# Optimization experiments

Measured on AMD Instinct MI355X. Metric: run time of the kernel, lower is better.

## Reference

```python
import jax, jax.numpy as jnp
import numpy as np

D_MODEL = 1024
N_HEADS = 16
D_HEAD = D_MODEL // N_HEADS
LN_EPS = 1e-5


def setup_inputs() -> dict:
    key = jax.random.key(0)
    ks = jax.random.split(key, 10)
    B, N = 2, 2048
    s = 1.0 / np.sqrt(D_MODEL)
    return {
        "x": jax.random.normal(ks[0], (B, N, D_MODEL), dtype=jnp.float32),
        "Wq": jax.random.normal(ks[1], (D_MODEL, D_MODEL), dtype=jnp.float32) * s,
        "bq": jnp.zeros((D_MODEL,), dtype=jnp.float32),
        "Wk": jax.random.normal(ks[2], (D_MODEL, D_MODEL), dtype=jnp.float32) * s,
        "bk": jnp.zeros((D_MODEL,), dtype=jnp.float32),
        "Wv": jax.random.normal(ks[3], (D_MODEL, D_MODEL), dtype=jnp.float32) * s,
        "bv": jnp.zeros((D_MODEL,), dtype=jnp.float32),
        "Wo": jax.random.normal(ks[4], (D_MODEL, D_MODEL), dtype=jnp.float32) * s,
        "bo": jnp.zeros((D_MODEL,), dtype=jnp.float32),
        "ln_gamma": jnp.ones((D_MODEL,), dtype=jnp.float32),
        "ln_beta": jnp.zeros((D_MODEL,), dtype=jnp.float32),
    }


def reference(x, Wq, bq, Wk, bk, Wv, bv, Wo, bo, ln_gamma, ln_beta):
    B, N, _ = x.shape
    # QKV projections -> [B, H, N, dh]
    def proj(W, b):
        return (x @ W.T + b).reshape(B, N, N_HEADS, D_HEAD).transpose(0, 2, 1, 3)
    Q, K, V = proj(Wq, bq), proj(Wk, bk), proj(Wv, bv)
    # scaled scores [B, H, N, N] with causal mask (is_mask=True)
    scores = jnp.einsum("bhqd,bhkd->bhqk", Q, K) / np.sqrt(D_HEAD)
    causal = jnp.tril(jnp.ones((N, N), dtype=bool))
    scores = jnp.where(causal, scores, -jnp.inf)
    attn = jax.nn.softmax(scores, axis=-1)  # dropout p=0 (eval)
    ctx = jnp.einsum("bhqk,bhkd->bhqd", attn, V)  # [B, H, N, dh]
    ctx = ctx.transpose(0, 2, 1, 3).reshape(B, N, D_MODEL)
    out = ctx @ Wo.T + bo + x  # output proj + residual
    # LayerNorm over last dim
    mu = out.mean(-1, keepdims=True)
    var = out.var(-1, keepdims=True)
    return (out - mu) / jnp.sqrt(var + LN_EPS) * ln_gamma + ln_beta
```

## Files before the change

kernel.cpp:

```cpp
#include <hip/hip_runtime.h>
#include <type_traits>

#define D_MODEL 1024
#define NHEADS 16
#define DHEAD 64
#define SEQ 2048
#define BATCH 2
#define MROWS (BATCH*SEQ)
#define NQT (SEQ/64)

typedef unsigned short ushort_t;
using bf16x8 = __attribute__((ext_vector_type(8))) __bf16;
using us4    = __attribute__((ext_vector_type(4))) unsigned short;
using us8    = __attribute__((ext_vector_type(8))) unsigned short;
using f32x4  = __attribute__((ext_vector_type(4))) float;

__device__ __forceinline__ ushort_t f2bf(float f) {
    unsigned int u = __builtin_bit_cast(unsigned int, f);
    u += 0x7FFFu + ((u >> 16) & 1u);
    return (ushort_t)(u >> 16);
}

__device__ __forceinline__ void gl2lds(const ushort_t* g, ushort_t* l) {
    __builtin_amdgcn_global_load_lds(
        (const __attribute__((address_space(1))) unsigned int*)g,
        (__attribute__((address_space(3))) unsigned int*)l,
        16, 0, 0);
}

__global__ __launch_bounds__(256) void cvt_kernel(
    const float* __restrict__ x,
    const float* __restrict__ wq, const float* __restrict__ wk,
    const float* __restrict__ wv, const float* __restrict__ wo,
    ushort_t* __restrict__ xb,
    ushort_t* __restrict__ wqb, ushort_t* __restrict__ wkb,
    ushort_t* __restrict__ wvb, ushort_t* __restrict__ wob)
{
    const size_t XN = (size_t)MROWS * D_MODEL;
    const size_t WN = (size_t)D_MODEL * D_MODEL;
    size_t i = ((size_t)blockIdx.x * 256 + threadIdx.x) * 4;
    const float* s; ushort_t* d; size_t off;
    if (i < XN) { s = x; d = xb; off = i; }
    else {
        size_t j = i - XN;
        int w = (int)(j / WN);
        off = j - (size_t)w * WN;
        s = (w == 0) ? wq : (w == 1) ? wk : (w == 2) ? wv : wo;
        d = (w == 0) ? wqb : (w == 1) ? wkb : (w == 2) ? wvb : wob;
    }
    const f32x4 v = *(const f32x4*)(s + off);
    us4 o;
    #pragma unroll
    for (int t = 0; t < 4; ++t) o[t] = f2bf(v[t]);
    *(us4*)(d + off) = o;
}

template<typename OutT, bool RES>
__global__ __launch_bounds__(256, 3) void gemm_nt(
    const ushort_t* __restrict__ A,
    const ushort_t* __restrict__ W0, const ushort_t* __restrict__ W1, const ushort_t* __restrict__ W2,
    const float* __restrict__ b0, const float* __restrict__ b1, const float* __restrict__ b2,
    const float* __restrict__ res,
    OutT* __restrict__ Y0, OutT* __restrict__ Y1, OutT* __restrict__ Y2)
{
    constexpr int K  = D_MODEL;
    constexpr int BK = 32;
    __shared__ ushort_t As[128 * BK];
    __shared__ ushort_t Ws[128 * BK];

    const int z = blockIdx.z;
    const ushort_t* W  = (z == 0) ? W0 : (z == 1) ? W1 : W2;
    const float* bias  = (z == 0) ? b0 : (z == 1) ? b1 : b2;
    OutT* Y            = (z == 0) ? Y0 : (z == 1) ? Y1 : Y2;

    const int i0 = blockIdx.x * 128;
    const int j0 = blockIdx.y * 128;
    const int tid  = threadIdx.x;
    const int lane = tid & 63;
    const int w    = tid >> 6;
    const int wm   = (w >> 1) * 64;
    const int wn   = (w & 1) * 64;
    const int l15  = lane & 15;
    const int quad = lane >> 4;

    const int srow = lane >> 2;
    const int scol = (lane & 3) * 8;
    const int c0 = w * 2, c1 = w * 2 + 1;
    const ushort_t* gA0 = A + (size_t)(i0 + c0 * 16 + srow) * K + scol;
    const ushort_t* gA1 = A + (size_t)(i0 + c1 * 16 + srow) * K + scol;
    const ushort_t* gW0 = W + (size_t)(j0 + c0 * 16 + srow) * K + scol;
    const ushort_t* gW1 = W + (size_t)(j0 + c1 * 16 + srow) * K + scol;
    ushort_t* lA0 = As + c0 * 512;
    ushort_t* lA1 = As + c1 * 512;
    ushort_t* lW0 = Ws + c0 * 512;
    ushort_t* lW1 = Ws + c1 * 512;

    f32x4 acc[4][4] = {};

    for (int k0 = 0; k0 < K; k0 += BK) {
        gl2lds(gA0 + k0, lA0);
        gl2lds(gA1 + k0, lA1);
        gl2lds(gW0 + k0, lW0);
        gl2lds(gW1 + k0, lW1);
        __syncthreads();

        bf16x8 af[4], wf[4];
        #pragma unroll
        for (int m = 0; m < 4; ++m)
            af[m] = *(const bf16x8*)&As[(wm + m * 16 + l15) * BK + quad * 8];
        #pragma unroll
        for (int n = 0; n < 4; ++n)
            wf[n] = *(const bf16x8*)&Ws[(wn + n * 16 + l15) * BK + quad * 8];
        #pragma unroll
        for (int m = 0; m < 4; ++m)
            #pragma unroll
            for (int n = 0; n < 4; ++n)
                acc[m][n] = __builtin_amdgcn_mfma_f32_16x16x32_bf16(af[m], wf[n], acc[m][n], 0, 0, 0);
        __syncthreads();
    }

    #pragma unroll
    for (int n = 0; n < 4; ++n) {
        const int col = j0 + wn + n * 16 + l15;
        const float bv = bias[col];
        #pragma unroll
        for (int m = 0; m < 4; ++m) {
            #pragma unroll
            for (int r = 0; r < 4; ++r) {
                const int row = i0 + wm + m * 16 + quad * 4 + r;
                float v = acc[m][n][r] + bv;
                if constexpr (RES) v += res[(size_t)row * D_MODEL + col];
                if constexpr (std::is_same<OutT, float>::value)
                    Y[(size_t)row * D_MODEL + col] = v;
                else
                    Y[(size_t)row * D_MODEL + col] = f2bf(v);
            }
        }
    }
}

#define VP 72

__global__ __launch_bounds__(256, 3) void attn_kernel(
    const ushort_t* __restrict__ Qg, const ushort_t* __restrict__ Kg,
    const ushort_t* __restrict__ Vg, ushort_t* __restrict__ Og)
{
    __shared__ ushort_t Kt[2][64 * VP];
    __shared__ ushort_t Vt[2][64 * VP];
    __shared__ ushort_t Pw[64 * VP];
    __shared__ ushort_t OnesR[16 * VP];

    const int bh = blockIdx.y;
    const int b = bh >> 4;
    const int h = bh & 15;
    const int p = blockIdx.x;
    const int tid  = threadIdx.x;
    const int lane = tid & 63;
    const int w    = tid >> 6;
    const int l15  = lane & 15;
    const int quad = lane >> 4;

    const size_t headoff = (size_t)h * DHEAD;
    const ushort_t* Kbase = Kg + (size_t)(b * SEQ) * D_MODEL + headoff;
    const ushort_t* Vbase = Vg + (size_t)(b * SEQ) * D_MODEL + headoff;

    const int krow = tid >> 3;
    const int kb   = tid & 7;
    const int vkey = tid & 63;
    const int dc0  = tid >> 6;
    const int dc1  = dc0 + 4;

    for (int i = tid; i < 16 * VP; i += 256) OnesR[i] = 0x3F80;

    bf16x8 onesf[2];
    bool onesLoaded = false;

    for (int half = 0; half < 2; ++half) {
        const int qt = half ? p : (NQT - 1 - p);
        const int q0 = qt * 64;
        const int qg = q0 + w * 16 + l15;
        const int nkt = qt + 1;

        const size_t qrow = (size_t)(b * SEQ + qg) * D_MODEL + headoff;
        const bf16x8 qf0 = *(const bf16x8*)&Qg[qrow + quad * 8];
        const bf16x8 qf1 = *(const bf16x8*)&Qg[qrow + 32 + quad * 8];

        float m_run = -1e30f;
        f32x4 o[4] = {};
        f32x4 o4 = {};

        us8 kp0, kp1, vp0, vp1;
        kp0 = *(const us8*)&Kbase[(size_t)krow * D_MODEL + kb * 8];
        kp1 = *(const us8*)&Kbase[(size_t)(32 + krow) * D_MODEL + kb * 8];
        vp0 = *(const us8*)&Vbase[(size_t)vkey * D_MODEL + dc0 * 8];
        vp1 = *(const us8*)&Vbase[(size_t)vkey * D_MODEL + dc1 * 8];
        *(us8*)&Kt[0][krow * VP + kb * 8]        = kp0;
        *(us8*)&Kt[0][(32 + krow) * VP + kb * 8] = kp1;
        #pragma unroll
        for (int j = 0; j < 8; ++j) {
            Vt[0][(dc0 * 8 + j) * VP + vkey] = vp0[j];
            Vt[0][(dc1 * 8 + j) * VP + vkey] = vp1[j];
        }
        __syncthreads();

        if (!onesLoaded) {
            onesf[0] = *(const bf16x8*)&OnesR[l15 * VP + quad * 8];
            onesf[1] = *(const bf16x8*)&OnesR[l15 * VP + 32 + quad * 8];
            onesLoaded = true;
        }

        for (int kt = 0; kt < nkt; ++kt) {
            const int cur = kt & 1;
            const int nxt = cur ^ 1;
            const bool pre = (kt + 1 < nkt);
            if (pre) {
                const size_t koff = (size_t)((kt + 1) * 64) * D_MODEL;
                kp0 = *(const us8*)&Kbase[koff + (size_t)krow * D_MODEL + kb * 8];
                kp1 = *(const us8*)&Kbase[koff + (size_t)(32 + krow) * D_MODEL + kb * 8];
                vp0 = *(const us8*)&Vbase[koff + (size_t)vkey * D_MODEL + dc0 * 8];
                vp1 = *(const us8*)&Vbase[koff + (size_t)vkey * D_MODEL + dc1 * 8];
            }

            f32x4 sv[4];
            #pragma unroll
            for (int f = 0; f < 4; ++f) {
                const bf16x8 kf0 = *(const bf16x8*)&Kt[cur][(f * 16 + l15) * VP + quad * 8];
                const bf16x8 kf1 = *(const bf16x8*)&Kt[cur][(f * 16 + l15) * VP + 32 + quad * 8];
                f32x4 s = {};
                s = __builtin_amdgcn_mfma_f32_16x16x32_bf16(kf0, qf0, s, 0, 0, 0);
                s = __builtin_amdgcn_mfma_f32_16x16x32_bf16(kf1, qf1, s, 0, 0, 0);
                sv[f] = s;
            }

            if (kt * 64 + 63 <= q0 + w * 16) {
                #pragma unroll
                for (int f = 0; f < 4; ++f)
                    #pragma unroll
                    for (int r = 0; r < 4; ++r) sv[f][r] *= 0.125f;
            } else {
                #pragma unroll
                for (int f = 0; f < 4; ++f) {
                    #pragma unroll
                    for (int r = 0; r < 4; ++r) {
                        const int kg = kt * 64 + f * 16 + quad * 4 + r;
                        sv[f][r] = (kg <= qg) ? sv[f][r] * 0.125f : -1e30f;
                    }
                }
            }

            float mf[4];
            #pragma unroll
            for (int f = 0; f < 4; ++f)
                mf[f] = fmaxf(fmaxf(sv[f][0], sv[f][1]), fmaxf(sv[f][2], sv[f][3]));
            float mx = fmaxf(fmaxf(mf[0], mf[1]), fmaxf(mf[2], mf[3]));
            mx = fmaxf(mx, __shfl_xor(mx, 16));
            mx = fmaxf(mx, __shfl_xor(mx, 32));
            const float mn = fmaxf(m_run, mx);
            const float al = __expf(m_run - mn);
            m_run = mn;
            #pragma unroll
            for (int f = 0; f < 4; ++f)
                #pragma unroll
                for (int r = 0; r < 4; ++r) sv[f][r] = __expf(sv[f][r] - mn);

            #pragma unroll
            for (int t = 0; t < 4; ++t)
                #pragma unroll
                for (int r = 0; r < 4; ++r) o[t][r] *= al;
            #pragma unroll
            for (int r = 0; r < 4; ++r) o4[r] *= al;

            #pragma unroll
            for (int f = 0; f < 4; ++f) {
                us4 pk;
                #pragma unroll
                for (int r = 0; r < 4; ++r) pk[r] = f2bf(sv[f][r]);
                *(us4*)&Pw[(w * 16 + l15) * VP + f * 16 + quad * 4] = pk;
            }
            __asm__ volatile("s_waitcnt lgkmcnt(0)" ::: "memory");

            #pragma unroll
            for (int s = 0; s < 2; ++s) {
                const bf16x8 pf = *(const bf16x8*)&Pw[(w * 16 + l15) * VP + s * 32 + quad * 8];
                #pragma unroll
                for (int t = 0; t < 4; ++t) {
                    const bf16x8 vf = *(const bf16x8*)&Vt[cur][(t * 16 + l15) * VP + s * 32 + quad * 8];
                    o[t] = __builtin_amdgcn_mfma_f32_16x16x32_bf16(vf, pf, o[t], 0, 0, 0);
                }
                o4 = __builtin_amdgcn_mfma_f32_16x16x32_bf16(onesf[s], pf, o4, 0, 0, 0);
            }

            if (pre) {
                *(us8*)&Kt[nxt][krow * VP + kb * 8]        = kp0;
                *(us8*)&Kt[nxt][(32 + krow) * VP + kb * 8] = kp1;
                #pragma unroll
                for (int j = 0; j < 8; ++j) {
                    Vt[nxt][(dc0 * 8 + j) * VP + vkey] = vp0[j];
                    Vt[nxt][(dc1 * 8 + j) * VP + vkey] = vp1[j];
                }
            }
            __asm__ volatile("s_waitcnt lgkmcnt(0)\n\ts_barrier" ::: "memory");
        }

        const float inv = 1.f / o4[0];
        const size_t orow = (size_t)(b * SEQ + q0 + w * 16 + l15) * D_MODEL + headoff;
        #pragma unroll
        for (int t = 0; t < 4; ++t) {
            us4 pk;
            #pragma unroll
            for (int r = 0; r < 4; ++r) pk[r] = f2bf(o[t][r] * inv);
            *(us4*)&Og[orow + t * 16 + quad * 4] = pk;
        }
    }
}

__global__ __launch_bounds__(256) void ln_kernel(
    const float* __restrict__ X, const float* __restrict__ g,
    const float* __restrict__ bta, float* __restrict__ out)
{
    __shared__ float r1[4], r2[4];
    const int row = blockIdx.x;
    const int tid = threadIdx.x;
    const float* p = X + (size_t)row * D_MODEL;
    float v[4]; float s1 = 0.f, s2 = 0.f;
    #pragma unroll
    for (int i = 0; i < 4; ++i) { v[i] = p[tid + 256 * i]; s1 += v[i]; s2 += v[i] * v[i]; }
    #pragma unroll
    for (int d = 32; d >= 1; d >>= 1) { s1 += __shfl_xor(s1, d); s2 += __shfl_xor(s2, d); }
    if ((tid & 63) == 0) { r1[tid >> 6] = s1; r2[tid >> 6] = s2; }
    __syncthreads();
    s1 = r1[0] + r1[1] + r1[2] + r1[3];
    s2 = r2[0] + r2[1] + r2[2] + r2[3];
    const float mu  = s1 * (1.f / D_MODEL);
    const float var = s2 * (1.f / D_MODEL) - mu * mu;
    const float rstd = rsqrtf(var + 1e-5f);
    #pragma unroll
    for (int i = 0; i < 4; ++i) {
        const int c = tid + 256 * i;
        out[(size_t)row * D_MODEL + c] = (v[i] - mu) * rstd * g[c] + bta[c];
    }
}

extern "C" void kernel_launch(void* const* d_in, const int* in_sizes, int n_in,
                              void* d_out, int out_size, void* d_ws, size_t ws_size,
                              hipStream_t stream) {
    const float* x     = (const float*)d_in[0];
    const float* Wq    = (const float*)d_in[1];
    const float* bq    = (const float*)d_in[2];
    const float* Wk    = (const float*)d_in[3];
    const float* bk    = (const float*)d_in[4];
    const float* Wv    = (const float*)d_in[5];
    const float* bv    = (const float*)d_in[6];
    const float* Wo    = (const float*)d_in[7];
    const float* bo    = (const float*)d_in[8];
    const float* gamma = (const float*)d_in[9];
    const float* beta  = (const float*)d_in[10];

    const size_t XN = (size_t)MROWS * D_MODEL;
    const size_t WN = (size_t)D_MODEL * D_MODEL;
    ushort_t* wsp = (ushort_t*)d_ws;
    ushort_t* xb  = wsp;
    ushort_t* Yq  = wsp + XN;
    ushort_t* Yk  = wsp + 2 * XN;
    ushort_t* Yv  = wsp + 3 * XN;
    ushort_t* Wqb = wsp + 4 * XN;
    ushort_t* Wkb = Wqb + WN;
    ushort_t* Wvb = Wkb + WN;
    ushort_t* Wob = Wvb + WN;
    ushort_t* ctx = xb;
    float*    pre = (float*)d_out;

    cvt_kernel<<<dim3(8192), 256, 0, stream>>>(x, Wq, Wk, Wv, Wo, xb, Wqb, Wkb, Wvb, Wob);

    gemm_nt<ushort_t, false><<<dim3(MROWS / 128, D_MODEL / 128, 3), 256, 0, stream>>>(
        xb, Wqb, Wkb, Wvb, bq, bk, bv, nullptr, Yq, Yk, Yv);

    attn_kernel<<<dim3(SEQ / 128, BATCH * NHEADS), 256, 0, stream>>>(Yq, Yk, Yv, ctx);

    gemm_nt<float, true><<<dim3(MROWS / 128, D_MODEL / 128, 1), 256, 0, stream>>>(
        ctx, Wob, Wob, Wob, bo, bo, bo, x, pre, pre, pre);

    ln_kernel<<<dim3(MROWS), 256, 0, stream>>>(pre, gamma, beta, (float*)d_out);
}
```

Baseline: 220.4 us.

## Process two key tiles per attention iteration with shared online-softmax rescale

Restructures the causal attention inner loop to handle two 64-key tiles per iteration. It computes both QK tiles, applies one max and rescale over both, then runs both PV products, and prefetches the next two tiles into registers. This halves the per-tile softmax rescale and reduction work and gives more independent MFMA work between barriers. In exchange it doubles the prefetch register footprint and adds a second barrier per iteration, which may cut occupancy under the launch bound of 3 blocks.

Measured after the change: 221.3 us. About the same (+0.4%).

```diff
diff --git a/kernel.cpp b/kernel.cpp
--- a/kernel.cpp
+++ b/kernel.cpp
@@ -141,13 +141,75 @@
 
 #define VP 72
 
+__device__ __forceinline__ void qk_tile(
+    const ushort_t* Ktb, const bf16x8& qf0, const bf16x8& qf1,
+    int l15, int quad, f32x4* sv)
+{
+    #pragma unroll
+    for (int f = 0; f < 4; ++f) {
+        const bf16x8 kf0 = *(const bf16x8*)&Ktb[(f * 16 + l15) * VP + quad * 8];
+        const bf16x8 kf1 = *(const bf16x8*)&Ktb[(f * 16 + l15) * VP + 32 + quad * 8];
+        f32x4 s = {};
+        s = __builtin_amdgcn_mfma_f32_16x16x32_bf16(kf0, qf0, s, 0, 0, 0);
+        s = __builtin_amdgcn_mfma_f32_16x16x32_bf16(kf1, qf1, s, 0, 0, 0);
+        sv[f] = s;
+    }
+}
+
+__device__ __forceinline__ void mask_scale(f32x4* sv, int kt, int q0w, int qg, int quad)
+{
+    if (kt * 64 + 63 <= q0w) {
+        #pragma unroll
+        for (int f = 0; f < 4; ++f)
+            #pragma unroll
+            for (int r = 0; r < 4; ++r) sv[f][r] *= 0.125f;
+    } else {
+        #pragma unroll
+        for (int f = 0; f < 4; ++f) {
+            #pragma unroll
+            for (int r = 0; r < 4; ++r) {
+                const int kg = kt * 64 + f * 16 + quad * 4 + r;
+                sv[f][r] = (kg <= qg) ? sv[f][r] * 0.125f : -1e30f;
+            }
+        }
+    }
+}
+
+__device__ __forceinline__ void pack_p(const f32x4* sv, ushort_t* PwX, int row, int quad)
+{
+    #pragma unroll
+    for (int f = 0; f < 4; ++f) {
+        us4 pk;
+        #pragma unroll
+        for (int r = 0; r < 4; ++r) pk[r] = f2bf(sv[f][r]);
+        *(us4*)&PwX[row * VP + f * 16 + quad * 4] = pk;
+    }
+}
+
+__device__ __forceinline__ void pv_tile(
+    const ushort_t* PwX, const ushort_t* Vtb, const bf16x8* onesf,
+    int row, int l15, int quad, f32x4 (&o)[4], f32x4& o4)
+{
+    #pragma unroll
+    for (int s = 0; s < 2; ++s) {
+        const bf16x8 pf = *(const bf16x8*)&PwX[row * VP + s * 32 + quad * 8];
+        #pragma unroll
+        for (int t = 0; t < 4; ++t) {
+            const bf16x8 vf = *(const bf16x8*)&Vtb[(t * 16 + l15) * VP + s * 32 + quad * 8];
+            o[t] = __builtin_amdgcn_mfma_f32_16x16x32_bf16(vf, pf, o[t], 0, 0, 0);
+        }
+        o4 = __builtin_amdgcn_mfma_f32_16x16x32_bf16(onesf[s], pf, o4, 0, 0, 0);
+    }
+}
+
 __global__ __launch_bounds__(256, 3) void attn_kernel(
     const ushort_t* __restrict__ Qg, const ushort_t* __restrict__ Kg,
     const ushort_t* __restrict__ Vg, ushort_t* __restrict__ Og)
 {
     __shared__ ushort_t Kt[2][64 * VP];
     __shared__ ushort_t Vt[2][64 * VP];
-    __shared__ ushort_t Pw[64 * VP];
+    __shared__ ushort_t Pw0[64 * VP];
+    __shared__ ushort_t Pw1[64 * VP];
     __shared__ ushort_t OnesR[16 * VP];
 
     const int bh = blockIdx.y;
@@ -172,6 +234,8 @@
 
     for (int i = tid; i < 16 * VP; i += 256) OnesR[i] = 0x3F80;
 
+    const int prow = w * 16 + l15;
+
     bf16x8 onesf[2];
     bool onesLoaded = false;
 
@@ -179,6 +243,7 @@
         const int qt = half ? p : (NQT - 1 - p);
         const int q0 = qt * 64;
         const int qg = q0 + w * 16 + l15;
+        const int q0w = q0 + w * 16;
         const int nkt = qt + 1;
 
         const size_t qrow = (size_t)(b * SEQ + qg) * D_MODEL + headoff;
@@ -189,17 +254,32 @@
         f32x4 o[4] = {};
         f32x4 o4 = {};
 
-        us8 kp0, kp1, vp0, vp1;
-        kp0 = *(const us8*)&Kbase[(size_t)krow * D_MODEL + kb * 8];
-        kp1 = *(const us8*)&Kbase[(size_t)(32 + krow) * D_MODEL + kb * 8];
-        vp0 = *(const us8*)&Vbase[(size_t)vkey * D_MODEL + dc0 * 8];
-        vp1 = *(const us8*)&Vbase[(size_t)vkey * D_MODEL + dc1 * 8];
-        *(us8*)&Kt[0][krow * VP + kb * 8]        = kp0;
-        *(us8*)&Kt[0][(32 + krow) * VP + kb * 8] = kp1;
-        #pragma unroll
-        for (int j = 0; j < 8; ++j) {
-            Vt[0][(dc0 * 8 + j) * VP + vkey] = vp0[j];
-            Vt[0][(dc1 * 8 + j) * VP + vkey] = vp1[j];
+        {
+            us8 k0 = *(const us8*)&Kbase[(size_t)krow * D_MODEL + kb * 8];
+            us8 k1 = *(const us8*)&Kbase[(size_t)(32 + krow) * D_MODEL + kb * 8];
+            us8 v0 = *(const us8*)&Vbase[(size_t)vkey * D_MODEL + dc0 * 8];
+            us8 v1 = *(const us8*)&Vbase[(size_t)vkey * D_MODEL + dc1 * 8];
+            *(us8*)&Kt[0][krow * VP + kb * 8]        = k0;
+            *(us8*)&Kt[0][(32 + krow) * VP + kb * 8] = k1;
+            #pragma unroll
+            for (int j = 0; j < 8; ++j) {
+                Vt[0][(dc0 * 8 + j) * VP + vkey] = v0[j];
+                Vt[0][(dc1 * 8 + j) * VP + vkey] = v1[j];
+            }
+            if (nkt > 1) {
+                const size_t koff = (size_t)64 * D_MODEL;
+                k0 = *(const us8*)&Kbase[koff + (size_t)krow * D_MODEL + kb * 8];
+                k1 = *(const us8*)&Kbase[koff + (size_t)(32 + krow) * D_MODEL + kb * 8];
+                v0 = *(const us8*)&Vbase[koff + (size_t)vkey * D_MODEL + dc0 * 8];
+                v1 = *(const us8*)&Vbase[koff + (size_t)vkey * D_MODEL + dc1 * 8];
+                *(us8*)&Kt[1][krow * VP + kb * 8]        = k0;
+                *(us8*)&Kt[1][(32 + krow) * VP + kb * 8] = k1;
+                #pragma unroll
+                for (int j = 0; j < 8; ++j) {
+                    Vt[1][(dc0 * 8 + j) * VP + vkey] = v0[j];
+                    Vt[1][(dc1 * 8 + j) * VP + vkey] = v1[j];
+                }
+            }
         }
         __syncthreads();
 
@@ -209,50 +289,38 @@
             onesLoaded = true;
         }
 
-        for (int kt = 0; kt < nkt; ++kt) {
-            const int cur = kt & 1;
-            const int nxt = cur ^ 1;
-            const bool pre = (kt + 1 < nkt);
-            if (pre) {
-                const size_t koff = (size_t)((kt + 1) * 64) * D_MODEL;
-                kp0 = *(const us8*)&Kbase[koff + (size_t)krow * D_MODEL + kb * 8];
-                kp1 = *(const us8*)&Kbase[koff + (size_t)(32 + krow) * D_MODEL + kb * 8];
-                vp0 = *(const us8*)&Vbase[koff + (size_t)vkey * D_MODEL + dc0 * 8];
-                vp1 = *(const us8*)&Vbase[koff + (size_t)vkey * D_MODEL + dc1 * 8];
-            }
-
-            f32x4 sv[4];
+        int kt = 0;
+        while (kt + 1 < nkt) {
+            const bool p0 = (kt + 2 < nkt);
+            const bool p1 = (kt + 3 < nkt);
+            us8 ka0, ka1, va0, va1, kb0_, kb1_, vb0, vb1;
+            if (p0) {
+                const size_t koff = (size_t)((kt + 2) * 64) * D_MODEL;
+                ka0 = *(const us8*)&Kbase[koff + (size_t)krow * D_MODEL + kb * 8];
+                ka1 = *(const us8*)&Kbase[koff + (size_t)(32 + krow) * D_MODEL + kb * 8];
+                va0 = *(const us8*)&Vbase[koff + (size_t)vkey * D_MODEL + dc0 * 8];
+                va1 = *(const us8*)&Vbase[koff + (size_t)vkey * D_MODEL + dc1 * 8];
+            }
+            if (p1) {
+                const size_t koff = (size_t)((kt + 3) * 64) * D_MODEL;
+                kb0_ = *(const us8*)&Kbase[koff + (size_t)krow * D_MODEL + kb * 8];
+                kb1_ = *(const us8*)&Kbase[koff + (size_t)(32 + krow) * D_MODEL + kb * 8];
+                vb0  = *(const us8*)&Vbase[koff + (size_t)vkey * D_MODEL + dc0 * 8];
+                vb1  = *(const us8*)&Vbase[koff + (size_t)vkey * D_MODEL + dc1 * 8];
+            }
+
+            f32x4 sv0[4], sv1[4];
+            qk_tile(Kt[0], qf0, qf1, l15, quad, sv0);
+            qk_tile(Kt[1], qf0, qf1, l15, quad, sv1);
+            mask_scale(sv0, kt,     q0w, qg, quad);
+            mask_scale(sv1, kt + 1, q0w, qg, quad);
+
+            float mx = -1e30f;
             #pragma unroll
             for (int f = 0; f < 4; ++f) {
-                const bf16x8 kf0 = *(const bf16x8*)&Kt[cur][(f * 16 + l15) * VP + quad * 8];
-                const bf16x8 kf1 = *(const bf16x8*)&Kt[cur][(f * 16 + l15) * VP + 32 + quad * 8];
-                f32x4 s = {};
-                s = __builtin_amdgcn_mfma_f32_16x16x32_bf16(kf0, qf0, s, 0, 0, 0);
-                s = __builtin_amdgcn_mfma_f32_16x16x32_bf16(kf1, qf1, s, 0, 0, 0);
-                sv[f] = s;
-            }
-
-            if (kt * 64 + 63 <= q0 + w * 16) {
-                #pragma unroll
-                for (int f = 0; f < 4; ++f)
-                    #pragma unroll
-                    for (int r = 0; r < 4; ++r) sv[f][r] *= 0.125f;
-            } else {
-                #pragma unroll
-                for (int f = 0; f < 4; ++f) {
-                    #pragma unroll
-                    for (int r = 0; r < 4; ++r) {
-                        const int kg = kt * 64 + f * 16 + quad * 4 + r;
-                        sv[f][r] = (kg <= qg) ? sv[f][r] * 0.125f : -1e30f;
-                    }
-                }
-            }
-
-            float mf[4];
-            #pragma unroll
-            for (int f = 0; f < 4; ++f)
-                mf[f] = fmaxf(fmaxf(sv[f][0], sv[f][1]), fmaxf(sv[f][2], sv[f][3]));
-            float mx = fmaxf(fmaxf(mf[0], mf[1]), fmaxf(mf[2], mf[3]));
+                mx = fmaxf(mx, fmaxf(fmaxf(sv0[f][0], sv0[f][1]), fmaxf(sv0[f][2], sv0[f][3])));
+                mx = fmaxf(mx, fmaxf(fmaxf(sv1[f][0], sv1[f][1]), fmaxf(sv1[f][2], sv1[f][3])));
+            }
             mx = fmaxf(mx, __shfl_xor(mx, 16));
             mx = fmaxf(mx, __shfl_xor(mx, 32));
             const float mn = fmaxf(m_run, mx);
@@ -261,8 +329,10 @@
             #pragma unroll
             for (int f = 0; f < 4; ++f)
                 #pragma unroll
-                for (int r = 0; r < 4; ++r) sv[f][r] = __expf(sv[f][r] - mn);
-
+                for (int r = 0; r < 4; ++r) {
+                    sv0[f][r] = __expf(sv0[f][r] - mn);
+                    sv1[f][r] = __expf(sv1[f][r] - mn);
+                }
             #pragma unroll
             for (int t = 0; t < 4; ++t)
                 #pragma unroll
@@ -270,35 +340,63 @@
             #pragma unroll
             for (int r = 0; r < 4; ++r) o4[r] *= al;
 
-            #pragma unroll
-            for (int f = 0; f < 4; ++f) {
-                us4 pk;
-                #pragma unroll
-                for (int r = 0; r < 4; ++r) pk[r] = f2bf(sv[f][r]);
-                *(us4*)&Pw[(w * 16 + l15) * VP + f * 16 + quad * 4] = pk;
-            }
+            pack_p(sv0, Pw0, prow, quad);
+            pack_p(sv1, Pw1, prow, quad);
             __asm__ volatile("s_waitcnt lgkmcnt(0)" ::: "memory");
 
-            #pragma unroll
-            for (int s = 0; s < 2; ++s) {
-                const bf16x8 pf = *(const bf16x8*)&Pw[(w * 16 + l15) * VP + s * 32 + quad * 8];
-                #pragma unroll
-                for (int t = 0; t < 4; ++t) {
-                    const bf16x8 vf = *(const bf16x8*)&Vt[cur][(t * 16 + l15) * VP + s * 32 + quad * 8];
-                    o[t] = __builtin_amdgcn_mfma_f32_16x16x32_bf16(vf, pf, o[t], 0, 0, 0);
+            pv_tile(Pw0, Vt[0], onesf, prow, l15, quad, o, o4);
+            pv_tile(Pw1, Vt[1], onesf, prow, l15, quad, o, o4);
+
+            __asm__ volatile("s_waitcnt lgkmcnt(0)\n\ts_barrier" ::: "memory");
+
+            if (p0) {
+                *(us8*)&Kt[0][krow * VP + kb * 8]        = ka0;
+                *(us8*)&Kt[0][(32 + krow) * VP + kb * 8] = ka1;
+                #pragma unroll
+                for (int j = 0; j < 8; ++j) {
+                    Vt[0][(dc0 * 8 + j) * VP + vkey] = va0[j];
+                    Vt[0][(dc1 * 8 + j) * VP + vkey] = va1[j];
                 }
-                o4 = __builtin_amdgcn_mfma_f32_16x16x32_bf16(onesf[s], pf, o4, 0, 0, 0);
-            }
-
-            if (pre) {
-                *(us8*)&Kt[nxt][krow * VP + kb * 8]        = kp0;
-                *(us8*)&Kt[nxt][(32 + krow) * VP + kb * 8] = kp1;
+            }
+            if (p1) {
+                *(us8*)&Kt[1][krow * VP + kb * 8]        = kb0_;
+                *(us8*)&Kt[1][(32 + krow) * VP + kb * 8] = kb1_;
                 #pragma unroll
                 for (int j = 0; j < 8; ++j) {
-                    Vt[nxt][(dc0 * 8 + j) * VP + vkey] = vp0[j];
-                    Vt[nxt][(dc1 * 8 + j) * VP + vkey] = vp1[j];
+                    Vt[1][(dc0 * 8 + j) * VP + vkey] = vb0[j];
+                    Vt[1][(dc1 * 8 + j) * VP + vkey] = vb1[j];
                 }
             }
+            __asm__ volatile("s_waitcnt lgkmcnt(0)\n\ts_barrier" ::: "memory");
+            kt += 2;
+        }
+        if (kt < nkt) {
+            f32x4 sv0[4];
+            qk_tile(Kt[0], qf0, qf1, l15, quad, sv0);
+            mask_scale(sv0, kt, q0w, qg, quad);
+            float mx = -1e30f;
+            #pragma unroll
+            for (int f = 0; f < 4; ++f)
+                mx = fmaxf(mx, fmaxf(fmaxf(sv0[f][0], sv0[f][1]), fmaxf(sv0[f][2], sv0[f][3])));
+            mx = fmaxf(mx, __shfl_xor(mx, 16));
+            mx = fmaxf(mx, __shfl_xor(mx, 32));
+            const float mn = fmaxf(m_run, mx);
+            const float al = __expf(m_run - mn);
+            m_run = mn;
+            #pragma unroll
+            for (int f = 0; f < 4; ++f)
+                #pragma unroll
+                for (int r = 0; r < 4; ++r) sv0[f][r] = __expf(sv0[f][r] - mn);
+            #pragma unroll
+            for (int t = 0; t < 4; ++t)
+                #pragma unroll
+                for (int r = 0; r < 4; ++r) o[t][r] *= al;
+            #pragma unroll
+            for (int r = 0; r < 4; ++r) o4[r] *= al;
+
+            pack_p(sv0, Pw0, prow, quad);
+            __asm__ volatile("s_waitcnt lgkmcnt(0)" ::: "memory");
+            pv_tile(Pw0, Vt[0], onesf, prow, l15, quad, o, o4);
             __asm__ volatile("s_waitcnt lgkmcnt(0)\n\ts_barrier" ::: "memory");
         }
 
```

## Widen GEMM K-step to 64 and vectorize epilogue via swapped MFMA operands

Applied to the files above, without the earlier changes.

The projection GEMM now loads two 32-wide K slices per iteration, which halves the number of barrier pairs across the K loop. The MFMA operands are swapped so each lane holds four consecutive output columns of one row. That lets the epilogue issue vectorized 16-byte float stores (or 8-byte bf16 stores), vector bias loads and vector residual loads in place of scalar strided ones. LDS use doubles per block, which may reduce occupancy under the 3-blocks-per-CU launch bound.

Result: no change. 218.2 us (-1.0%).

```diff
diff --git a/kernel.cpp b/kernel.cpp
--- a/kernel.cpp
+++ b/kernel.cpp
@@ -63,10 +63,9 @@
     const float* __restrict__ res,
     OutT* __restrict__ Y0, OutT* __restrict__ Y1, OutT* __restrict__ Y2)
 {
-    constexpr int K  = D_MODEL;
-    constexpr int BK = 32;
-    __shared__ ushort_t As[128 * BK];
-    __shared__ ushort_t Ws[128 * BK];
+    constexpr int K = D_MODEL;
+    __shared__ ushort_t As[2][128 * 32];
+    __shared__ ushort_t Ws[2][128 * 32];
 
     const int z = blockIdx.z;
     const ushort_t* W  = (z == 0) ? W0 : (z == 1) ? W1 : W2;
@@ -90,50 +89,60 @@
     const ushort_t* gA1 = A + (size_t)(i0 + c1 * 16 + srow) * K + scol;
     const ushort_t* gW0 = W + (size_t)(j0 + c0 * 16 + srow) * K + scol;
     const ushort_t* gW1 = W + (size_t)(j0 + c1 * 16 + srow) * K + scol;
-    ushort_t* lA0 = As + c0 * 512;
-    ushort_t* lA1 = As + c1 * 512;
-    ushort_t* lW0 = Ws + c0 * 512;
-    ushort_t* lW1 = Ws + c1 * 512;
 
     f32x4 acc[4][4] = {};
 
-    for (int k0 = 0; k0 < K; k0 += BK) {
-        gl2lds(gA0 + k0, lA0);
-        gl2lds(gA1 + k0, lA1);
-        gl2lds(gW0 + k0, lW0);
-        gl2lds(gW1 + k0, lW1);
+    for (int k0 = 0; k0 < K; k0 += 64) {
+        gl2lds(gA0 + k0,      &As[0][c0 * 512]);
+        gl2lds(gA1 + k0,      &As[0][c1 * 512]);
+        gl2lds(gA0 + k0 + 32, &As[1][c0 * 512]);
+        gl2lds(gA1 + k0 + 32, &As[1][c1 * 512]);
+        gl2lds(gW0 + k0,      &Ws[0][c0 * 512]);
+        gl2lds(gW1 + k0,      &Ws[0][c1 * 512]);
+        gl2lds(gW0 + k0 + 32, &Ws[1][c0 * 512]);
+        gl2lds(gW1 + k0 + 32, &Ws[1][c1 * 512]);
         __syncthreads();
 
-        bf16x8 af[4], wf[4];
         #pragma unroll
-        for (int m = 0; m < 4; ++m)
-            af[m] = *(const bf16x8*)&As[(wm + m * 16 + l15) * BK + quad * 8];
-        #pragma unroll
-        for (int n = 0; n < 4; ++n)
-            wf[n] = *(const bf16x8*)&Ws[(wn + n * 16 + l15) * BK + quad * 8];
-        #pragma unroll
-        for (int m = 0; m < 4; ++m)
+        for (int s = 0; s < 2; ++s) {
+            bf16x8 af[4], wf[4];
+            #pragma unroll
+            for (int m = 0; m < 4; ++m)
+                af[m] = *(const bf16x8*)&As[s][(wm + m * 16 + l15) * 32 + quad * 8];
             #pragma unroll
             for (int n = 0; n < 4; ++n)
-                acc[m][n] = __builtin_amdgcn_mfma_f32_16x16x32_bf16(af[m], wf[n], acc[m][n], 0, 0, 0);
+                wf[n] = *(const bf16x8*)&Ws[s][(wn + n * 16 + l15) * 32 + quad * 8];
+            #pragma unroll
+            for (int m = 0; m < 4; ++m)
+                #pragma unroll
+                for (int n = 0; n < 4; ++n)
+                    acc[m][n] = __builtin_amdgcn_mfma_f32_16x16x32_bf16(wf[n], af[m], acc[m][n], 0, 0, 0);
+        }
         __syncthreads();
     }
 
     #pragma unroll
     for (int n = 0; n < 4; ++n) {
-        const int col = j0 + wn + n * 16 + l15;
-        const float bv = bias[col];
+        const int col = j0 + wn + n * 16 + quad * 4;
+        const f32x4 bv = *(const f32x4*)&bias[col];
         #pragma unroll
         for (int m = 0; m < 4; ++m) {
-            #pragma unroll
-            for (int r = 0; r < 4; ++r) {
-                const int row = i0 + wm + m * 16 + quad * 4 + r;
-                float v = acc[m][n][r] + bv;
-                if constexpr (RES) v += res[(size_t)row * D_MODEL + col];
-                if constexpr (std::is_same<OutT, float>::value)
-                    Y[(size_t)row * D_MODEL + col] = v;
-                else
-                    Y[(size_t)row * D_MODEL + col] = f2bf(v);
+            const int row = i0 + wm + m * 16 + l15;
+            if constexpr (std::is_same<OutT, float>::value) {
+                f32x4 v;
+                #pragma unroll
+                for (int r = 0; r < 4; ++r) v[r] = acc[m][n][r] + bv[r];
+                if constexpr (RES) {
+                    const f32x4 rv = *(const f32x4*)&res[(size_t)row * D_MODEL + col];
+                    #pragma unroll
+                    for (int r = 0; r < 4; ++r) v[r] += rv[r];
+                }
+                *(f32x4*)&Y[(size_t)row * D_MODEL + col] = v;
+            } else {
+                us4 pk;
+                #pragma unroll
+                for (int r = 0; r < 4; ++r) pk[r] = f2bf(acc[m][n][r] + bv[r]);
+                *(us4*)&Y[(size_t)row * D_MODEL + col] = pk;
             }
         }
     }
```
